# Kernel optimization log

Hardware: AMD Instinct MI355X
Metric: run time of the kernel (lower is better)

Reference implementation:

```python
import jax, jax.numpy as jnp
import numpy as np

D_MODEL, D_STATE, D_CONV, EXPAND = 512, 16, 4, 2
D_INNER = EXPAND * D_MODEL
DT_RANK = -(-D_MODEL // 16)  # ceil(512/16) = 32
B, L = 1, 2048


def setup_inputs() -> dict:
    key = jax.random.key(0)
    ks = jax.random.split(key, 10)
    x = jax.random.normal(ks[0], (B, L, D_MODEL), dtype=jnp.float32)
    in_proj_w = jax.random.normal(ks[1], (2 * D_INNER, D_MODEL), dtype=jnp.float32) * (D_MODEL ** -0.5)
    conv_w = jax.random.normal(ks[2], (D_INNER, 1, D_CONV), dtype=jnp.float32) * (D_CONV ** -0.5)
    conv_b = jax.random.normal(ks[3], (D_INNER,), dtype=jnp.float32) * 0.02
    x_proj_w = jax.random.normal(ks[4], (DT_RANK + 2 * D_STATE, D_INNER), dtype=jnp.float32) * (D_INNER ** -0.5)
    dt_init_std = DT_RANK ** -0.5
    dt_proj_w = jax.random.uniform(ks[5], (D_INNER, DT_RANK), minval=-dt_init_std, maxval=dt_init_std, dtype=jnp.float32)
    # dt bias init: inverse-softplus of dt sampled log-uniform in [dt_min, dt_max]
    dt = jnp.exp(jax.random.uniform(ks[6], (D_INNER,)) * (np.log(0.1) - np.log(0.001)) + np.log(0.001))
    dt = jnp.clip(dt, 1e-4, None)
    dt_proj_b = dt + jnp.log(-jnp.expm1(-dt))
    A_log = jnp.log(jnp.broadcast_to(jnp.arange(1, D_STATE + 1, dtype=jnp.float32), (D_INNER, D_STATE)))
    D = jnp.ones((D_INNER,), dtype=jnp.float32)
    out_proj_w = jax.random.normal(ks[7], (D_MODEL, D_INNER), dtype=jnp.float32) * (D_INNER ** -0.5)
    return {"x": x, "in_proj_w": in_proj_w, "conv_w": conv_w, "conv_b": conv_b,
            "x_proj_w": x_proj_w, "dt_proj_w": dt_proj_w, "dt_proj_b": dt_proj_b,
            "A_log": A_log, "D": D, "out_proj_w": out_proj_w}


def _selective_scan_parallel(x, deltaA, deltaB, C):
    # x: (B,L,D)  deltaA/deltaB: (B,L,D,N)  C: (B,L,N)
    log_dA = jnp.log(jnp.clip(deltaA, 1e-6, None))
    cum_dA = jnp.exp(jnp.cumsum(log_dA, axis=1))                      # (B,L,D,N)
    Bx = deltaB * x[..., None]                                        # (B,L,D,N)
    cum_dA_prev = jnp.concatenate([jnp.ones_like(cum_dA[:, :1]), cum_dA[:, :-1]], axis=1)
    h = cum_dA * jnp.cumsum(Bx / (cum_dA_prev + 1e-8), axis=1)        # (B,L,D,N)
    return jnp.einsum('bldn,bln->bld', h, C)


def reference(x, in_proj_w, conv_w, conv_b, x_proj_w, dt_proj_w, dt_proj_b, A_log, D, out_proj_w):
    xz = jnp.einsum('bld,ed->ble', x, in_proj_w)            # (B,L,2*D_inner)
    xp, z = jnp.split(xz, 2, axis=-1)
    # causal depthwise conv1d: left-pad d_conv-1, groups = d_inner
    xc = jax.lax.conv_general_dilated(
        jnp.transpose(xp, (0, 2, 1)), conv_w, window_strides=(1,),
        padding=[(D_CONV - 1, 0)], dimension_numbers=('NCH', 'OIH', 'NCH'),
        feature_group_count=D_INNER) + conv_b[None, :, None]
    xp = jax.nn.silu(jnp.transpose(xc, (0, 2, 1)))          # (B,L,D_inner)
    # SSM
    A = -jnp.exp(A_log.astype(jnp.float32))                 # (D_inner, N)
    x_dbl = jnp.einsum('bld,ed->ble', xp, x_proj_w)
    delta, Bm, Cm = jnp.split(x_dbl, [DT_RANK, DT_RANK + D_STATE], axis=-1)
    delta = jax.nn.softplus(jnp.einsum('blr,dr->bld', delta, dt_proj_w) + dt_proj_b)
    deltaA = jnp.exp(delta[..., None] * A)                  # (B,L,D,N)
    deltaB = delta[..., None] * Bm[:, :, None, :]           # (B,L,D,N)
    y = _selective_scan_parallel(xp, deltaA, deltaB, Cm)
    y = y + xp * D
    out = y * jax.nn.silu(z)
    return jnp.einsum('bld,md->blm', out, out_proj_w)
```

## Files before the change

kernel.cpp:

```cpp
#include <hip/hip_runtime.h>
#include <hip/hip_bf16.h>

#define L_SEQ   2048
#define D_MODEL 512
#define D_INNER 1024
#define D_STATE 16
#define DT_RANK 32

typedef unsigned short u16;
typedef short bf16x8 __attribute__((ext_vector_type(8)));
typedef float f32x4  __attribute__((ext_vector_type(4)));
typedef unsigned short u16x8 __attribute__((ext_vector_type(8)));

__device__ __forceinline__ u16 f2bf(float f) {
    union { float f; unsigned u; } x; x.f = f;
    unsigned r = x.u + 0x7FFFu + ((x.u >> 16) & 1u);
    return (u16)(r >> 16);
}

__device__ __forceinline__ void gload_lds16(const void* g, void* l) {
    __builtin_amdgcn_global_load_lds((const __attribute__((address_space(1))) void*)g,
                                     (__attribute__((address_space(3))) void*)l, 16, 0, 0);
}

template<int BM, int BN>
__global__ __launch_bounds__(256)
void gemm_mfma_nt(const u16* __restrict__ A, const u16* __restrict__ B,
                  float* __restrict__ C, int M, int N, int K, int ldc) {
    constexpr int FM = BM / 32;
    constexpr int FN = BN / 32;
    __shared__ u16 lA[BM * 64];
    __shared__ u16 lB[BN * 64];

    const int tid  = threadIdx.x;
    const int lane = tid & 63;
    const int w    = tid >> 6;
    const int wr   = w >> 1, wc = w & 1;
    const int m0 = blockIdx.y * BM;
    const int n0 = blockIdx.x * BN;

    f32x4 acc[FM][FN];
#pragma unroll
    for (int m = 0; m < FM; m++)
#pragma unroll
        for (int n = 0; n < FN; n++) acc[m][n] = (f32x4){0.f, 0.f, 0.f, 0.f};

    int offA[FM][2], offB[FN][2];
#pragma unroll
    for (int m = 0; m < FM; m++) {
        int r = wr * (BM / 2) + m * 16 + (lane & 15);
#pragma unroll
        for (int s = 0; s < 2; s++) {
            int kb = s * 4 + (lane >> 4);
            offA[m][s] = r * 128 + ((kb ^ (r & 7)) << 4);
        }
    }
#pragma unroll
    for (int n = 0; n < FN; n++) {
        int r = wc * (BN / 2) + n * 16 + (lane & 15);
#pragma unroll
        for (int s = 0; s < 2; s++) {
            int kb = s * 4 + (lane >> 4);
            offB[n][s] = r * 128 + ((kb ^ (r & 7)) << 4);
        }
    }

    const int ldsbase = (tid & 192) * 16;

    for (int k0 = 0; k0 < K; k0 += 64) {
        __syncthreads();
#pragma unroll
        for (int i = 0; i < BM / 32; i++) {
            int o = i * 4096 + tid * 16;
            int r = o >> 7;
            int kb = ((o >> 4) & 7) ^ (r & 7);
            gload_lds16(A + (size_t)(m0 + r) * K + k0 + kb * 8,
                        (char*)lA + i * 4096 + ldsbase);
        }
#pragma unroll
        for (int i = 0; i < BN / 32; i++) {
            int o = i * 4096 + tid * 16;
            int r = o >> 7;
            int kb = ((o >> 4) & 7) ^ (r & 7);
            gload_lds16(B + (size_t)(n0 + r) * K + k0 + kb * 8,
                        (char*)lB + i * 4096 + ldsbase);
        }
        __syncthreads();

#pragma unroll
        for (int s = 0; s < 2; s++) {
            bf16x8 av[FM], bv[FN];
#pragma unroll
            for (int m = 0; m < FM; m++)
                av[m] = *(const bf16x8*)((const char*)lA + offA[m][s]);
#pragma unroll
            for (int n = 0; n < FN; n++)
                bv[n] = *(const bf16x8*)((const char*)lB + offB[n][s]);
#pragma unroll
            for (int m = 0; m < FM; m++)
#pragma unroll
                for (int n = 0; n < FN; n++)
                    acc[m][n] = __builtin_amdgcn_mfma_f32_16x16x32_bf16(
                        av[m], bv[n], acc[m][n], 0, 0, 0);
        }
    }

    const int rb = (lane >> 4) * 4;
    const int cb = lane & 15;
#pragma unroll
    for (int m = 0; m < FM; m++)
#pragma unroll
        for (int n = 0; n < FN; n++) {
            int col = n0 + wc * (BN / 2) + n * 16 + cb;
#pragma unroll
            for (int j = 0; j < 4; j++) {
                int row = m0 + wr * (BM / 2) + m * 16 + rb + j;
                C[(size_t)row * ldc + col] = acc[m][n][j];
            }
        }
}

__global__ __launch_bounds__(256)
void cast3_kernel(const float* __restrict__ x, const float* __restrict__ w1,
                  const float* __restrict__ w2,
                  u16* __restrict__ xb, u16* __restrict__ w1b, u16* __restrict__ w2b) {
    int g = blockIdx.x * 256 + threadIdx.x;
    const float* src; u16* dst; int off;
    if (g < 131072)      { src = x;  dst = xb;  off = g; }
    else if (g < 262144) { src = w1; dst = w1b; off = g - 131072; }
    else                 { src = w2; dst = w2b; off = g - 262144; }
    float4 v0 = ((const float4*)src)[off * 2];
    float4 v1 = ((const float4*)src)[off * 2 + 1];
    u16x8 r;
    r[0] = f2bf(v0.x); r[1] = f2bf(v0.y); r[2] = f2bf(v0.z); r[3] = f2bf(v0.w);
    r[4] = f2bf(v1.x); r[5] = f2bf(v1.y); r[6] = f2bf(v1.z); r[7] = f2bf(v1.w);
    *(u16x8*)(dst + (size_t)off * 8) = r;
}

__global__ __launch_bounds__(256)
void conv_rows_kernel(const float* __restrict__ xzT,
                      const float* __restrict__ w,
                      const float* __restrict__ b,
                      float* __restrict__ xpcT) {
    const int d = blockIdx.y;
    const int l = blockIdx.x * 1024 + threadIdx.x * 4;
    const float4 wv = ((const float4*)w)[d];
    const float bias = b[d];
    const float* row = xzT + (size_t)d * L_SEQ;

    float4 cur  = *(const float4*)(row + l);
    float4 prev = (l == 0) ? make_float4(0.f, 0.f, 0.f, 0.f)
                           : *(const float4*)(row + l - 4);
    float e1 = prev.y, e2 = prev.z, e3 = prev.w;
    float e4 = cur.x, e5 = cur.y, e6 = cur.z, e7 = cur.w;
    float4 r;
    r.x = bias + wv.x * e1 + wv.y * e2 + wv.z * e3 + wv.w * e4;
    r.y = bias + wv.x * e2 + wv.y * e3 + wv.z * e4 + wv.w * e5;
    r.z = bias + wv.x * e3 + wv.y * e4 + wv.z * e5 + wv.w * e6;
    r.w = bias + wv.x * e4 + wv.y * e5 + wv.z * e6 + wv.w * e7;
    r.x = r.x / (1.f + __expf(-r.x));
    r.y = r.y / (1.f + __expf(-r.y));
    r.z = r.z / (1.f + __expf(-r.z));
    r.w = r.w / (1.f + __expf(-r.w));
    *(float4*)(xpcT + (size_t)d * L_SEQ + l) = r;
}

__global__ __launch_bounds__(256)
void xproj_kernel(const float* __restrict__ xpcT,
                  const float* __restrict__ xw,
                  float* __restrict__ xdblT) {
    const int tid  = threadIdx.x;
    const int part = tid >> 7;
    const int e    = (tid >> 1) & 63;
    const int lc   = tid & 1;
    const int l0   = blockIdx.x * 8;

    const float* wrow = xw + (size_t)e * 1024 + part * 512;
    const float* xcol = xpcT + (size_t)part * 512 * L_SEQ + l0 + lc * 4;

    f32x4 acc = {0.f, 0.f, 0.f, 0.f};
#pragma unroll 4
    for (int k = 0; k < 512; k += 4) {
        float4 wv = *(const float4*)(wrow + k);
        f32x4 x0 = *(const f32x4*)(xcol + (size_t)(k + 0) * L_SEQ);
        f32x4 x1 = *(const f32x4*)(xcol + (size_t)(k + 1) * L_SEQ);
        f32x4 x2 = *(const f32x4*)(xcol + (size_t)(k + 2) * L_SEQ);
        f32x4 x3 = *(const f32x4*)(xcol + (size_t)(k + 3) * L_SEQ);
        acc += wv.x * x0 + wv.y * x1 + wv.z * x2 + wv.w * x3;
    }

    __shared__ f32x4 red[128];
    if (part == 1) red[(e << 1) | lc] = acc;
    __syncthreads();
    if (part == 0) {
        acc += red[(e << 1) | lc];
        *(f32x4*)(xdblT + (size_t)e * L_SEQ + l0 + lc * 4) = acc;
    }
}

__global__ __launch_bounds__(256)
void deltaT_kernel(const float* __restrict__ xdblT,
                   const float* __restrict__ dtw,
                   const float* __restrict__ dtb,
                   float* __restrict__ deltaT) {
    const int tid = threadIdx.x;
    const int d0 = blockIdx.x * 64;
    const int l0 = blockIdx.y * 128;

    __shared__ float sx[32][128];
#pragma unroll
    for (int it = 0; it < 4; it++) {
        int idx = it * 256 + tid;
        int r  = idx >> 5;
        int c4 = (idx & 31) * 4;
        *(float4*)&sx[r][c4] = *(const float4*)(xdblT + (size_t)r * 2048 + l0 + c4);
    }

    const int dl = tid >> 2;
    const int lg = tid & 3;
    const int d  = d0 + dl;
    float wreg[32];
#pragma unroll
    for (int r4 = 0; r4 < 32; r4 += 4)
        *(float4*)&wreg[r4] = *(const float4*)(dtw + (size_t)d * 32 + r4);
    const float bias = dtb[d];
    __syncthreads();

#pragma unroll
    for (int j = 0; j < 8; j++) {
        float4 a = make_float4(bias, bias, bias, bias);
        const int col = j * 16 + lg * 4;
#pragma unroll
        for (int r = 0; r < 32; r++) {
            float4 v = *(const float4*)&sx[r][col];
            a.x = fmaf(wreg[r], v.x, a.x);
            a.y = fmaf(wreg[r], v.y, a.y);
            a.z = fmaf(wreg[r], v.z, a.z);
            a.w = fmaf(wreg[r], v.w, a.w);
        }
        float4 o;
        o.x = fmaxf(a.x, 0.f) + log1pf(expf(-fabsf(a.x)));
        o.y = fmaxf(a.y, 0.f) + log1pf(expf(-fabsf(a.y)));
        o.z = fmaxf(a.z, 0.f) + log1pf(expf(-fabsf(a.z)));
        o.w = fmaxf(a.w, 0.f) + log1pf(expf(-fabsf(a.w)));
        *(float4*)(deltaT + (size_t)d * 2048 + l0 + col) = o;
    }
}

#define NCHUNK 32

__global__ __launch_bounds__(1024)
void scan_kernel(const float* __restrict__ deltaT,
                 const float* __restrict__ xpcT,
                 const float* __restrict__ xzT,
                 const float* __restrict__ xdblT,
                 const float* __restrict__ A_log, const float* __restrict__ Dv,
                 u16* __restrict__ ypre) {
    const int tid   = threadIdx.x;
    const int lane  = tid & 63;
    const int chunk = ((tid >> 6) << 1) | (lane >> 5);
    const int dl    = (lane >> 4) & 1;
    const int n     = lane & 15;
    const int li    = (dl << 4) | n;
    const int d0    = blockIdx.x * 2;
    const int d     = d0 + dl;
    const int lb    = chunk * 64;

    const float Aneg = -__expf(A_log[d * D_STATE + n]);
    const float Dd   = Dv[d];

    const f32x4* dT4 = (const f32x4*)(deltaT + (size_t)d * L_SEQ + lb);
    const f32x4* xT4 = (const f32x4*)(xpcT   + (size_t)d * L_SEQ + lb);
    const f32x4* zT4 = (const f32x4*)(xzT    + (size_t)(1024 + d) * L_SEQ + lb);
    const f32x4* bT4 = (const f32x4*)(xdblT + (size_t)(32 + n) * L_SEQ + lb);
    const f32x4* cT4 = (const f32x4*)(xdblT + (size_t)(48 + n) * L_SEQ + lb);

    __shared__ float sLog[NCHUNK][32];
    __shared__ float sP[NCHUNK][32];
    __shared__ float sH[NCHUNK][32];
    __shared__ float s_y[L_SEQ][2];

    const float clipLog = -13.815511f;
    float s = 0.f;
#pragma unroll 8
    for (int i = 0; i < 16; i++) {
        f32x4 d4 = dT4[i];
#pragma unroll
        for (int k = 0; k < 4; k++) s += fmaxf(d4[k] * Aneg, clipLog);
    }
    sLog[chunk][li] = s;
    sP[chunk][li]   = __expf(s);
    __syncthreads();

    float lsum = 0.f;
    for (int v = 0; v < chunk; v++) lsum += sLog[v][li];
    const float cAs = __expf(lsum);

    float hloc = 0.f, cA = cAs;
    for (int i = 0; i < 16; i++) {
        f32x4 d4 = dT4[i], x4 = xT4[i], b4 = bT4[i];
#pragma unroll
        for (int k = 0; k < 4; k++) {
            float dA = fmaxf(__expf(d4[k] * Aneg), 1e-6f);
            float g  = cA * __builtin_amdgcn_rcpf(cA + 1e-8f);
            hloc = dA * hloc + (dA * g) * (d4[k] * b4[k] * x4[k]);
            cA *= dA;
        }
    }
    sH[chunk][li] = hloc;
    __syncthreads();

    float h = 0.f;
    for (int v = 0; v < chunk; v++) h = sP[v][li] * h + sH[v][li];

    cA = cAs;
    for (int i = 0; i < 16; i++) {
        f32x4 d4 = dT4[i], x4 = xT4[i], b4 = bT4[i], c4 = cT4[i];
        f32x4 z4 = zT4[i];
#pragma unroll
        for (int k = 0; k < 4; k++) {
            float dA = fmaxf(__expf(d4[k] * Aneg), 1e-6f);
            float g  = cA * __builtin_amdgcn_rcpf(cA + 1e-8f);
            h  = dA * h + (dA * g) * (d4[k] * b4[k] * x4[k]);
            cA *= dA;
            float p = h * c4[k];
            p += __shfl_xor(p, 1);
            p += __shfl_xor(p, 2);
            p += __shfl_xor(p, 4);
            p += __shfl_xor(p, 8);
            if (n == 0) {
                float sz = z4[k] * __builtin_amdgcn_rcpf(1.f + __expf(-z4[k]));
                s_y[lb + 4 * i + k][dl] = (p + x4[k] * Dd) * sz;
            }
        }
    }
    __syncthreads();

    for (int l = tid; l < L_SEQ; l += 1024) {
        ushort2 o;
        o.x = f2bf(s_y[l][0]);
        o.y = f2bf(s_y[l][1]);
        *(ushort2*)(ypre + (size_t)l * D_INNER + d0) = o;
    }
}

extern "C" void kernel_launch(void* const* d_in, const int* in_sizes, int n_in,
                              void* d_out, int out_size, void* d_ws, size_t ws_size,
                              hipStream_t stream) {
    const float* x          = (const float*)d_in[0];
    const float* in_proj_w  = (const float*)d_in[1];
    const float* conv_w     = (const float*)d_in[2];
    const float* conv_b     = (const float*)d_in[3];
    const float* x_proj_w   = (const float*)d_in[4];
    const float* dt_proj_w  = (const float*)d_in[5];
    const float* dt_proj_b  = (const float*)d_in[6];
    const float* A_log      = (const float*)d_in[7];
    const float* Dv         = (const float*)d_in[8];
    const float* out_proj_w = (const float*)d_in[9];
    float* out = (float*)d_out;
    float* ws  = (float*)d_ws;

    float* xzT    = ws;
    float* xpcT   = ws + 4194304;
    float* deltaT = ws + 6291456;
    float* xdblT  = ws + 8388608;
    u16*   ypre   = (u16*)(ws + 8519680);
    u16*   xb     = (u16*)(ws + 9568256);
    u16*   w1b    = (u16*)(ws + 10092544);
    u16*   w2b    = (u16*)(ws + 10616832);

    cast3_kernel<<<1280, 256, 0, stream>>>(x, in_proj_w, out_proj_w, xb, w1b, w2b);

    gemm_mfma_nt<128, 128><<<dim3(2048 / 128, 2048 / 128), 256, 0, stream>>>(
        w1b, xb, xzT, 2 * D_INNER, L_SEQ, D_MODEL, L_SEQ);

    conv_rows_kernel<<<dim3(2, 1024), 256, 0, stream>>>(xzT, conv_w, conv_b, xpcT);

    xproj_kernel<<<256, 256, 0, stream>>>(xpcT, x_proj_w, xdblT);

    deltaT_kernel<<<dim3(16, 16), 256, 0, stream>>>(xdblT, dt_proj_w, dt_proj_b,
                                                    deltaT);

    scan_kernel<<<512, 1024, 0, stream>>>(deltaT, xpcT, xzT, xdblT,
                                          A_log, Dv, ypre);

    gemm_mfma_nt<64, 64><<<dim3(512 / 64, 2048 / 64), 256, 0, stream>>>(
        ypre, w2b, out, L_SEQ, D_MODEL, D_INNER, D_MODEL);
}
```

Measured before the change: 167.8 us.

## Fuse dt projection into scan, batch shuffle reductions, transpose output separately

Removes the separate deltaT kernel: each scan block now computes softplus(dt_proj) for its two channels into shared memory, which avoids the deltaT global round trip. The per-step 4-stage shuffle reduction of h*C is replaced by a batched transpose-reduce over 16 timesteps, cutting shuffle count. The scan now writes y in a channel-major bf16 layout with coalesced stores, and a new tile transpose kernel converts it to row-major for the output GEMM. Launch bounds also request 4 waves per SIMD. The cost is redundant dt_proj work across blocks sharing xdblT and an extra kernel launch plus transpose traffic.

```diff
diff --git a/kernel.cpp b/kernel.cpp
--- a/kernel.cpp
+++ b/kernel.cpp
@@ -198,64 +198,16 @@
     }
 }
 
-__global__ __launch_bounds__(256)
-void deltaT_kernel(const float* __restrict__ xdblT,
-                   const float* __restrict__ dtw,
-                   const float* __restrict__ dtb,
-                   float* __restrict__ deltaT) {
-    const int tid = threadIdx.x;
-    const int d0 = blockIdx.x * 64;
-    const int l0 = blockIdx.y * 128;
-
-    __shared__ float sx[32][128];
-#pragma unroll
-    for (int it = 0; it < 4; it++) {
-        int idx = it * 256 + tid;
-        int r  = idx >> 5;
-        int c4 = (idx & 31) * 4;
-        *(float4*)&sx[r][c4] = *(const float4*)(xdblT + (size_t)r * 2048 + l0 + c4);
-    }
-
-    const int dl = tid >> 2;
-    const int lg = tid & 3;
-    const int d  = d0 + dl;
-    float wreg[32];
-#pragma unroll
-    for (int r4 = 0; r4 < 32; r4 += 4)
-        *(float4*)&wreg[r4] = *(const float4*)(dtw + (size_t)d * 32 + r4);
-    const float bias = dtb[d];
-    __syncthreads();
-
-#pragma unroll
-    for (int j = 0; j < 8; j++) {
-        float4 a = make_float4(bias, bias, bias, bias);
-        const int col = j * 16 + lg * 4;
-#pragma unroll
-        for (int r = 0; r < 32; r++) {
-            float4 v = *(const float4*)&sx[r][col];
-            a.x = fmaf(wreg[r], v.x, a.x);
-            a.y = fmaf(wreg[r], v.y, a.y);
-            a.z = fmaf(wreg[r], v.z, a.z);
-            a.w = fmaf(wreg[r], v.w, a.w);
-        }
-        float4 o;
-        o.x = fmaxf(a.x, 0.f) + log1pf(expf(-fabsf(a.x)));
-        o.y = fmaxf(a.y, 0.f) + log1pf(expf(-fabsf(a.y)));
-        o.z = fmaxf(a.z, 0.f) + log1pf(expf(-fabsf(a.z)));
-        o.w = fmaxf(a.w, 0.f) + log1pf(expf(-fabsf(a.w)));
-        *(float4*)(deltaT + (size_t)d * 2048 + l0 + col) = o;
-    }
-}
-
 #define NCHUNK 32
 
-__global__ __launch_bounds__(1024)
-void scan_kernel(const float* __restrict__ deltaT,
-                 const float* __restrict__ xpcT,
+__global__ __launch_bounds__(1024, 4)
+void scan_kernel(const float* __restrict__ xpcT,
                  const float* __restrict__ xzT,
                  const float* __restrict__ xdblT,
+                 const float* __restrict__ dtw,
+                 const float* __restrict__ dtb,
                  const float* __restrict__ A_log, const float* __restrict__ Dv,
-                 u16* __restrict__ ypre) {
+                 u16* __restrict__ ypreT) {
     const int tid   = threadIdx.x;
     const int lane  = tid & 63;
     const int chunk = ((tid >> 6) << 1) | (lane >> 5);
@@ -266,25 +218,44 @@
     const int d     = d0 + dl;
     const int lb    = chunk * 64;
 
-    const float Aneg = -__expf(A_log[d * D_STATE + n]);
-    const float Dd   = Dv[d];
-
-    const f32x4* dT4 = (const f32x4*)(deltaT + (size_t)d * L_SEQ + lb);
-    const f32x4* xT4 = (const f32x4*)(xpcT   + (size_t)d * L_SEQ + lb);
-    const f32x4* zT4 = (const f32x4*)(xzT    + (size_t)(1024 + d) * L_SEQ + lb);
-    const f32x4* bT4 = (const f32x4*)(xdblT + (size_t)(32 + n) * L_SEQ + lb);
-    const f32x4* cT4 = (const f32x4*)(xdblT + (size_t)(48 + n) * L_SEQ + lb);
-
+    __shared__ float sDelta[2][L_SEQ];
+    __shared__ float s_y[2][L_SEQ];
     __shared__ float sLog[NCHUNK][32];
     __shared__ float sP[NCHUNK][32];
     __shared__ float sH[NCHUNK][32];
-    __shared__ float s_y[L_SEQ][2];
+
+    {
+        const int pdl = tid >> 9;
+        const int pl  = (tid & 511) * 4;
+        const int pd  = d0 + pdl;
+        float wreg[32];
+#pragma unroll
+        for (int r = 0; r < 32; r += 4)
+            *(float4*)&wreg[r] = *(const float4*)(dtw + (size_t)pd * 32 + r);
+        const float bias = dtb[pd];
+        f32x4 a = {bias, bias, bias, bias};
+#pragma unroll 8
+        for (int r = 0; r < 32; r++) {
+            f32x4 xv = *(const f32x4*)(xdblT + (size_t)r * L_SEQ + pl);
+            a += wreg[r] * xv;
+        }
+        f32x4 o;
+#pragma unroll
+        for (int k = 0; k < 4; k++)
+            o[k] = fmaxf(a[k], 0.f) + log1pf(expf(-fabsf(a[k])));
+        *(f32x4*)&sDelta[pdl][pl] = o;
+    }
+    __syncthreads();
+
+    const float Aneg = -__expf(A_log[d * D_STATE + n]);
+    const float Dd   = Dv[d];
+    const f32x4* dls = (const f32x4*)&sDelta[dl][lb];
 
     const float clipLog = -13.815511f;
     float s = 0.f;
-#pragma unroll 8
+#pragma unroll 4
     for (int i = 0; i < 16; i++) {
-        f32x4 d4 = dT4[i];
+        f32x4 d4 = dls[i];
 #pragma unroll
         for (int k = 0; k < 4; k++) s += fmaxf(d4[k] * Aneg, clipLog);
     }
@@ -296,9 +267,14 @@
     for (int v = 0; v < chunk; v++) lsum += sLog[v][li];
     const float cAs = __expf(lsum);
 
+    const f32x4* xT4 = (const f32x4*)(xpcT  + (size_t)d * L_SEQ + lb);
+    const f32x4* bT4 = (const f32x4*)(xdblT + (size_t)(32 + n) * L_SEQ + lb);
+    const f32x4* cT4 = (const f32x4*)(xdblT + (size_t)(48 + n) * L_SEQ + lb);
+
     float hloc = 0.f, cA = cAs;
+#pragma unroll 4
     for (int i = 0; i < 16; i++) {
-        f32x4 d4 = dT4[i], x4 = xT4[i], b4 = bT4[i];
+        f32x4 d4 = dls[i], x4 = xT4[i], b4 = bT4[i];
 #pragma unroll
         for (int k = 0; k < 4; k++) {
             float dA = fmaxf(__expf(d4[k] * Aneg), 1e-6f);
@@ -314,33 +290,67 @@
     for (int v = 0; v < chunk; v++) h = sP[v][li] * h + sH[v][li];
 
     cA = cAs;
-    for (int i = 0; i < 16; i++) {
-        f32x4 d4 = dT4[i], x4 = xT4[i], b4 = bT4[i], c4 = cT4[i];
-        f32x4 z4 = zT4[i];
-#pragma unroll
-        for (int k = 0; k < 4; k++) {
-            float dA = fmaxf(__expf(d4[k] * Aneg), 1e-6f);
-            float g  = cA * __builtin_amdgcn_rcpf(cA + 1e-8f);
-            h  = dA * h + (dA * g) * (d4[k] * b4[k] * x4[k]);
-            cA *= dA;
-            float p = h * c4[k];
-            p += __shfl_xor(p, 1);
-            p += __shfl_xor(p, 2);
-            p += __shfl_xor(p, 4);
-            p += __shfl_xor(p, 8);
-            if (n == 0) {
-                float sz = z4[k] * __builtin_amdgcn_rcpf(1.f + __expf(-z4[k]));
-                s_y[lb + 4 * i + k][dl] = (p + x4[k] * Dd) * sz;
+    const float* xrow = xpcT + (size_t)d * L_SEQ;
+    const float* zrow = xzT + (size_t)(1024 + d) * L_SEQ;
+#pragma unroll 1
+    for (int b = 0; b < 4; b++) {
+        float v[16];
+#pragma unroll
+        for (int i = 0; i < 4; i++) {
+            const int idx = b * 4 + i;
+            f32x4 d4 = dls[idx], x4 = xT4[idx], b4 = bT4[idx], c4 = cT4[idx];
+#pragma unroll
+            for (int k = 0; k < 4; k++) {
+                float dA = fmaxf(__expf(d4[k] * Aneg), 1e-6f);
+                float g  = cA * __builtin_amdgcn_rcpf(cA + 1e-8f);
+                h  = dA * h + (dA * g) * (d4[k] * b4[k] * x4[k]);
+                cA *= dA;
+                v[i * 4 + k] = h * c4[k];
             }
         }
-    }
-    __syncthreads();
-
-    for (int l = tid; l < L_SEQ; l += 1024) {
-        ushort2 o;
-        o.x = f2bf(s_y[l][0]);
-        o.y = f2bf(s_y[l][1]);
-        *(ushort2*)(ypre + (size_t)l * D_INNER + d0) = o;
+#pragma unroll
+        for (int m = 8; m >= 1; m >>= 1) {
+#pragma unroll
+            for (int j = 0; j < m; j++) {
+                float send = (n & m) ? v[j] : v[j + m];
+                float keep = (n & m) ? v[j + m] : v[j];
+                v[j] = keep + __shfl_xor(send, m);
+            }
+        }
+        const int t = lb + b * 16 + n;
+        float xv = xrow[t];
+        float zv = zrow[t];
+        float sz = zv * __builtin_amdgcn_rcpf(1.f + __expf(-zv));
+        s_y[dl][t] = (v[0] + xv * Dd) * sz;
+    }
+    __syncthreads();
+
+    {
+        const int rdl = tid >> 9;
+        const int pos = (tid & 511) * 4;
+        f32x4 v = *(const f32x4*)&s_y[rdl][pos];
+        ushort4 o;
+        o.x = f2bf(v[0]); o.y = f2bf(v[1]); o.z = f2bf(v[2]); o.w = f2bf(v[3]);
+        *(ushort4*)(ypreT + (size_t)(d0 + rdl) * L_SEQ + pos) = o;
+    }
+}
+
+__global__ __launch_bounds__(256)
+void trans_bf16_kernel(const u16* __restrict__ src, u16* __restrict__ dst) {
+    __shared__ u16 t[64][72];
+    const int d0 = blockIdx.x * 64, l0 = blockIdx.y * 64;
+    const int r = threadIdx.x >> 3;
+    const int c = (threadIdx.x & 7) * 8;
+#pragma unroll
+    for (int rr = r; rr < 64; rr += 32)
+        *(u16x8*)&t[rr][c] = *(const u16x8*)(src + (size_t)(d0 + rr) * L_SEQ + l0 + c);
+    __syncthreads();
+#pragma unroll
+    for (int rr = r; rr < 64; rr += 32) {
+        u16x8 v;
+#pragma unroll
+        for (int j = 0; j < 8; j++) v[j] = t[c + j][rr];
+        *(u16x8*)(dst + (size_t)(l0 + rr) * D_INNER + d0 + c) = v;
     }
 }
 
@@ -362,12 +372,12 @@
 
     float* xzT    = ws;
     float* xpcT   = ws + 4194304;
-    float* deltaT = ws + 6291456;
-    float* xdblT  = ws + 8388608;
-    u16*   ypre   = (u16*)(ws + 8519680);
-    u16*   xb     = (u16*)(ws + 9568256);
-    u16*   w1b    = (u16*)(ws + 10092544);
-    u16*   w2b    = (u16*)(ws + 10616832);
+    float* xdblT  = ws + 6291456;
+    u16*   ypreT  = (u16*)(ws + 6422528);
+    u16*   ypre   = (u16*)(ws + 7471104);
+    u16*   xb     = (u16*)(ws + 8519680);
+    u16*   w1b    = (u16*)(ws + 9043968);
+    u16*   w2b    = (u16*)(ws + 9568256);
 
     cast3_kernel<<<1280, 256, 0, stream>>>(x, in_proj_w, out_proj_w, xb, w1b, w2b);
 
@@ -378,11 +388,10 @@
 
     xproj_kernel<<<256, 256, 0, stream>>>(xpcT, x_proj_w, xdblT);
 
-    deltaT_kernel<<<dim3(16, 16), 256, 0, stream>>>(xdblT, dt_proj_w, dt_proj_b,
-                                                    deltaT);
-
-    scan_kernel<<<512, 1024, 0, stream>>>(deltaT, xpcT, xzT, xdblT,
-                                          A_log, Dv, ypre);
+    scan_kernel<<<512, 1024, 0, stream>>>(xpcT, xzT, xdblT, dt_proj_w, dt_proj_b,
+                                          A_log, Dv, ypreT);
+
+    trans_bf16_kernel<<<dim3(16, 32), 256, 0, stream>>>(ypreT, ypre);
 
     gemm_mfma_nt<64, 64><<<dim3(512 / 64, 2048 / 64), 256, 0, stream>>>(
         ypre, w2b, out, L_SEQ, D_MODEL, D_INNER, D_MODEL);
```

Result: slower. 204.8 us (+22.0%).

## Scan one channel per block with 64 chunks, transpose output separately, retile GEMMs

Applied to the files above, without the earlier changes.

The scan kernel now gives each block a single inner channel and splits the sequence into 64 chunks of 32 steps instead of 32 chunks of 64 across two channels. This doubles the block count and shortens the serial per-thread loops. The output is written channel-major with contiguous stores, and a new bf16 transpose kernel builds the row-major input for the out-projection GEMM. The in-projection GEMM moves to 64x64 tiles and the out-projection to 64x32 tiles for more blocks. This adds a kernel launch and an extra pass over the intermediate, and z is now loaded as a scalar by one lane per step.

```diff
diff --git a/kernel.cpp b/kernel.cpp
--- a/kernel.cpp
+++ b/kernel.cpp
@@ -247,7 +247,8 @@
     }
 }
 
-#define NCHUNK 32
+#define NCH 64
+#define CK  32
 
 __global__ __launch_bounds__(1024)
 void scan_kernel(const float* __restrict__ deltaT,
@@ -255,49 +256,46 @@
                  const float* __restrict__ xzT,
                  const float* __restrict__ xdblT,
                  const float* __restrict__ A_log, const float* __restrict__ Dv,
-                 u16* __restrict__ ypre) {
+                 u16* __restrict__ ypreT) {
     const int tid   = threadIdx.x;
     const int lane  = tid & 63;
-    const int chunk = ((tid >> 6) << 1) | (lane >> 5);
-    const int dl    = (lane >> 4) & 1;
+    const int chunk = ((tid >> 6) << 2) | (lane >> 4);
     const int n     = lane & 15;
-    const int li    = (dl << 4) | n;
-    const int d0    = blockIdx.x * 2;
-    const int d     = d0 + dl;
-    const int lb    = chunk * 64;
+    const int d     = blockIdx.x;
+    const int lb    = chunk * CK;
 
     const float Aneg = -__expf(A_log[d * D_STATE + n]);
     const float Dd   = Dv[d];
 
     const f32x4* dT4 = (const f32x4*)(deltaT + (size_t)d * L_SEQ + lb);
     const f32x4* xT4 = (const f32x4*)(xpcT   + (size_t)d * L_SEQ + lb);
-    const f32x4* zT4 = (const f32x4*)(xzT    + (size_t)(1024 + d) * L_SEQ + lb);
     const f32x4* bT4 = (const f32x4*)(xdblT + (size_t)(32 + n) * L_SEQ + lb);
     const f32x4* cT4 = (const f32x4*)(xdblT + (size_t)(48 + n) * L_SEQ + lb);
 
-    __shared__ float sLog[NCHUNK][32];
-    __shared__ float sP[NCHUNK][32];
-    __shared__ float sH[NCHUNK][32];
-    __shared__ float s_y[L_SEQ][2];
+    __shared__ float sLog[NCH][16];
+    __shared__ float sP[NCH][16];
+    __shared__ float sH[NCH][16];
+    __shared__ float s_y[L_SEQ];
 
     const float clipLog = -13.815511f;
     float s = 0.f;
-#pragma unroll 8
-    for (int i = 0; i < 16; i++) {
+#pragma unroll
+    for (int i = 0; i < CK / 4; i++) {
         f32x4 d4 = dT4[i];
 #pragma unroll
         for (int k = 0; k < 4; k++) s += fmaxf(d4[k] * Aneg, clipLog);
     }
-    sLog[chunk][li] = s;
-    sP[chunk][li]   = __expf(s);
+    sLog[chunk][n] = s;
+    sP[chunk][n]   = __expf(s);
     __syncthreads();
 
     float lsum = 0.f;
-    for (int v = 0; v < chunk; v++) lsum += sLog[v][li];
+    for (int v = 0; v < chunk; v++) lsum += sLog[v][n];
     const float cAs = __expf(lsum);
 
     float hloc = 0.f, cA = cAs;
-    for (int i = 0; i < 16; i++) {
+#pragma unroll 4
+    for (int i = 0; i < CK / 4; i++) {
         f32x4 d4 = dT4[i], x4 = xT4[i], b4 = bT4[i];
 #pragma unroll
         for (int k = 0; k < 4; k++) {
@@ -307,16 +305,17 @@
             cA *= dA;
         }
     }
-    sH[chunk][li] = hloc;
+    sH[chunk][n] = hloc;
     __syncthreads();
 
     float h = 0.f;
-    for (int v = 0; v < chunk; v++) h = sP[v][li] * h + sH[v][li];
+    for (int v = 0; v < chunk; v++) h = sP[v][n] * h + sH[v][n];
 
     cA = cAs;
-    for (int i = 0; i < 16; i++) {
+    const float* zrow = xzT + (size_t)(1024 + d) * L_SEQ;
+#pragma unroll 4
+    for (int i = 0; i < CK / 4; i++) {
         f32x4 d4 = dT4[i], x4 = xT4[i], b4 = bT4[i], c4 = cT4[i];
-        f32x4 z4 = zT4[i];
 #pragma unroll
         for (int k = 0; k < 4; k++) {
             float dA = fmaxf(__expf(d4[k] * Aneg), 1e-6f);
@@ -329,18 +328,40 @@
             p += __shfl_xor(p, 4);
             p += __shfl_xor(p, 8);
             if (n == 0) {
-                float sz = z4[k] * __builtin_amdgcn_rcpf(1.f + __expf(-z4[k]));
-                s_y[lb + 4 * i + k][dl] = (p + x4[k] * Dd) * sz;
+                const int t = lb + 4 * i + k;
+                float zv = zrow[t];
+                float sz = zv * __builtin_amdgcn_rcpf(1.f + __expf(-zv));
+                s_y[t] = (p + x4[k] * Dd) * sz;
             }
         }
     }
     __syncthreads();
 
-    for (int l = tid; l < L_SEQ; l += 1024) {
+    {
+        float2 v = *(const float2*)&s_y[tid * 2];
         ushort2 o;
-        o.x = f2bf(s_y[l][0]);
-        o.y = f2bf(s_y[l][1]);
-        *(ushort2*)(ypre + (size_t)l * D_INNER + d0) = o;
+        o.x = f2bf(v.x);
+        o.y = f2bf(v.y);
+        *(ushort2*)(ypreT + (size_t)d * L_SEQ + tid * 2) = o;
+    }
+}
+
+__global__ __launch_bounds__(256)
+void trans_bf16_kernel(const u16* __restrict__ src, u16* __restrict__ dst) {
+    __shared__ u16 t[64][72];
+    const int d0 = blockIdx.x * 64, l0 = blockIdx.y * 64;
+    const int r = threadIdx.x >> 3;
+    const int c = (threadIdx.x & 7) * 8;
+#pragma unroll
+    for (int rr = r; rr < 64; rr += 32)
+        *(u16x8*)&t[rr][c] = *(const u16x8*)(src + (size_t)(d0 + rr) * L_SEQ + l0 + c);
+    __syncthreads();
+#pragma unroll
+    for (int rr = r; rr < 64; rr += 32) {
+        u16x8 v;
+#pragma unroll
+        for (int j = 0; j < 8; j++) v[j] = t[c + j][rr];
+        *(u16x8*)(dst + (size_t)(l0 + rr) * D_INNER + d0 + c) = v;
     }
 }
 
@@ -362,16 +383,17 @@
 
     float* xzT    = ws;
     float* xpcT   = ws + 4194304;
-    float* deltaT = ws + 6291456;
-    float* xdblT  = ws + 8388608;
-    u16*   ypre   = (u16*)(ws + 8519680);
-    u16*   xb     = (u16*)(ws + 9568256);
-    u16*   w1b    = (u16*)(ws + 10092544);
-    u16*   w2b    = (u16*)(ws + 10616832);
+    float* xdblT  = ws + 6291456;
+    float* deltaT = ws + 6422528;
+    u16*   ypreT  = (u16*)(ws + 8519680);
+    u16*   ypre   = (u16*)(ws + 9568256);
+    u16*   xb     = (u16*)(ws + 10616832);
+    u16*   w1b    = (u16*)(ws + 11141120);
+    u16*   w2b    = (u16*)(ws + 11665408);
 
     cast3_kernel<<<1280, 256, 0, stream>>>(x, in_proj_w, out_proj_w, xb, w1b, w2b);
 
-    gemm_mfma_nt<128, 128><<<dim3(2048 / 128, 2048 / 128), 256, 0, stream>>>(
+    gemm_mfma_nt<64, 64><<<dim3(2048 / 64, 2048 / 64), 256, 0, stream>>>(
         w1b, xb, xzT, 2 * D_INNER, L_SEQ, D_MODEL, L_SEQ);
 
     conv_rows_kernel<<<dim3(2, 1024), 256, 0, stream>>>(xzT, conv_w, conv_b, xpcT);
@@ -381,9 +403,11 @@
     deltaT_kernel<<<dim3(16, 16), 256, 0, stream>>>(xdblT, dt_proj_w, dt_proj_b,
                                                     deltaT);
 
-    scan_kernel<<<512, 1024, 0, stream>>>(deltaT, xpcT, xzT, xdblT,
-                                          A_log, Dv, ypre);
-
-    gemm_mfma_nt<64, 64><<<dim3(512 / 64, 2048 / 64), 256, 0, stream>>>(
+    scan_kernel<<<1024, 1024, 0, stream>>>(deltaT, xpcT, xzT, xdblT,
+                                           A_log, Dv, ypreT);
+
+    trans_bf16_kernel<<<dim3(16, 32), 256, 0, stream>>>(ypreT, ypre);
+
+    gemm_mfma_nt<64, 32><<<dim3(512 / 32, 2048 / 64), 256, 0, stream>>>(
         ypre, w2b, out, L_SEQ, D_MODEL, D_INNER, D_MODEL);
 }
```

New measurement: 219.6 us. 1.31x slower.

## Write scan output transposed, add bf16 transpose kernel, retune GEMM tiles

Applied to the files above, without the earlier changes.

The scan kernel now stores its output as a transposed bf16 buffer with contiguous 4-element vector stores, in place of scattered 4-byte writes strided across rows. A separate LDS-tiled transpose kernel converts that buffer back to row-major for the output projection. The in_proj GEMM tile drops from 128x128 to 64x64 and the out_proj GEMM uses 64x32 tiles, which gives more blocks for occupancy. The cost is an extra kernel launch and an extra pass over the bf16 intermediate.

```diff
diff --git a/kernel.cpp b/kernel.cpp
--- a/kernel.cpp
+++ b/kernel.cpp
@@ -255,7 +255,7 @@
                  const float* __restrict__ xzT,
                  const float* __restrict__ xdblT,
                  const float* __restrict__ A_log, const float* __restrict__ Dv,
-                 u16* __restrict__ ypre) {
+                 u16* __restrict__ ypreT) {
     const int tid   = threadIdx.x;
     const int lane  = tid & 63;
     const int chunk = ((tid >> 6) << 1) | (lane >> 5);
@@ -278,7 +278,7 @@
     __shared__ float sLog[NCHUNK][32];
     __shared__ float sP[NCHUNK][32];
     __shared__ float sH[NCHUNK][32];
-    __shared__ float s_y[L_SEQ][2];
+    __shared__ float s_y[2][L_SEQ];
 
     const float clipLog = -13.815511f;
     float s = 0.f;
@@ -330,17 +330,38 @@
             p += __shfl_xor(p, 8);
             if (n == 0) {
                 float sz = z4[k] * __builtin_amdgcn_rcpf(1.f + __expf(-z4[k]));
-                s_y[lb + 4 * i + k][dl] = (p + x4[k] * Dd) * sz;
+                s_y[dl][lb + 4 * i + k] = (p + x4[k] * Dd) * sz;
             }
         }
     }
     __syncthreads();
 
-    for (int l = tid; l < L_SEQ; l += 1024) {
-        ushort2 o;
-        o.x = f2bf(s_y[l][0]);
-        o.y = f2bf(s_y[l][1]);
-        *(ushort2*)(ypre + (size_t)l * D_INNER + d0) = o;
+    {
+        const int rdl = tid >> 9;
+        const int pos = (tid & 511) * 4;
+        f32x4 v = *(const f32x4*)&s_y[rdl][pos];
+        ushort4 o;
+        o.x = f2bf(v[0]); o.y = f2bf(v[1]); o.z = f2bf(v[2]); o.w = f2bf(v[3]);
+        *(ushort4*)(ypreT + (size_t)(d0 + rdl) * L_SEQ + pos) = o;
+    }
+}
+
+__global__ __launch_bounds__(256)
+void trans_bf16_kernel(const u16* __restrict__ src, u16* __restrict__ dst) {
+    __shared__ u16 t[64][72];
+    const int d0 = blockIdx.x * 64, l0 = blockIdx.y * 64;
+    const int r = threadIdx.x >> 3;
+    const int c = (threadIdx.x & 7) * 8;
+#pragma unroll
+    for (int rr = r; rr < 64; rr += 32)
+        *(u16x8*)&t[rr][c] = *(const u16x8*)(src + (size_t)(d0 + rr) * L_SEQ + l0 + c);
+    __syncthreads();
+#pragma unroll
+    for (int rr = r; rr < 64; rr += 32) {
+        u16x8 v;
+#pragma unroll
+        for (int j = 0; j < 8; j++) v[j] = t[c + j][rr];
+        *(u16x8*)(dst + (size_t)(l0 + rr) * D_INNER + d0 + c) = v;
     }
 }
 
@@ -362,16 +383,17 @@
 
     float* xzT    = ws;
     float* xpcT   = ws + 4194304;
-    float* deltaT = ws + 6291456;
-    float* xdblT  = ws + 8388608;
-    u16*   ypre   = (u16*)(ws + 8519680);
-    u16*   xb     = (u16*)(ws + 9568256);
-    u16*   w1b    = (u16*)(ws + 10092544);
-    u16*   w2b    = (u16*)(ws + 10616832);
+    float* xdblT  = ws + 6291456;
+    float* deltaT = ws + 6422528;
+    u16*   ypreT  = (u16*)(ws + 8519680);
+    u16*   ypre   = (u16*)(ws + 9568256);
+    u16*   xb     = (u16*)(ws + 10616832);
+    u16*   w1b    = (u16*)(ws + 11141120);
+    u16*   w2b    = (u16*)(ws + 11665408);
 
     cast3_kernel<<<1280, 256, 0, stream>>>(x, in_proj_w, out_proj_w, xb, w1b, w2b);
 
-    gemm_mfma_nt<128, 128><<<dim3(2048 / 128, 2048 / 128), 256, 0, stream>>>(
+    gemm_mfma_nt<64, 64><<<dim3(2048 / 64, 2048 / 64), 256, 0, stream>>>(
         w1b, xb, xzT, 2 * D_INNER, L_SEQ, D_MODEL, L_SEQ);
 
     conv_rows_kernel<<<dim3(2, 1024), 256, 0, stream>>>(xzT, conv_w, conv_b, xpcT);
@@ -382,8 +404,10 @@
                                                     deltaT);
 
     scan_kernel<<<512, 1024, 0, stream>>>(deltaT, xpcT, xzT, xdblT,
-                                          A_log, Dv, ypre);
-
-    gemm_mfma_nt<64, 64><<<dim3(512 / 64, 2048 / 64), 256, 0, stream>>>(
+                                          A_log, Dv, ypreT);
+
+    trans_bf16_kernel<<<dim3(16, 32), 256, 0, stream>>>(ypreT, ypre);
+
+    gemm_mfma_nt<64, 32><<<dim3(512 / 32, 2048 / 64), 256, 0, stream>>>(
         ypre, w2b, out, L_SEQ, D_MODEL, D_INNER, D_MODEL);
 }
```

After: 158.4 us. 5.6% less time.
